# Kernel tuning notes

Hardware: AMD Instinct MI355X
Metric: run time of the kernel (lower is better)

Reference implementation:

```python
import jax, jax.numpy as jnp
import numpy as np

SR = 44100        # sample rate (init arg)
WIN = 442         # FFT window length from tensor[i:i+442]
HOP = 4           # loop stride
NBINS = 221       # kept spectrum bins x[:221]
THR = 0.01        # threshold passed to inner fftLayer
REL = 0.0594      # relative pitch-change threshold
BIN_HZ = 100.0    # argmax*100 -> frequency


def _windows_and_mag(tensor):
    n = tensor.shape[0]
    n_win = (n - WIN + HOP - 1) // HOP
    starts = jnp.arange(n_win) * HOP
    windows = tensor[starts[:, None] + jnp.arange(WIN)[None, :]]
    spec = jnp.fft.fft(windows, axis=-1)[:, :NBINS]           # complex64 [n_win, 221]
    spec = jnp.where(jnp.abs(spec) < THR, jnp.zeros_like(spec), spec)  # fftLayer threshold
    mag = jnp.abs(spec.real) + jnp.abs(spec.imag)             # |re| + |im|, as in forward
    return mag, starts


def setup_inputs() -> dict:
    key = jax.random.key(0)
    return {"tensor": jax.random.normal(key, (1_000_000,), dtype=jnp.float32)}


def reference(tensor):
    mag, starts = _windows_and_mag(tensor)
    # per-window dominant frequency: argmax bin * 100 Hz
    tmp = jnp.argmax(mag, axis=-1).astype(jnp.float32) * BIN_HZ    # [n_win]
    i_samp = starts.astype(jnp.float32)                            # sample index of each window

    def step(carry, x):
        maxF, Ftime = carry
        t, i = x
        cond = jnp.abs(maxF - t) > maxF * REL
        emit_f = maxF
        emit_d = (i - Ftime) * 1000.0 / SR
        maxF = jnp.where(cond, t, maxF)
        Ftime = jnp.where(cond, i, Ftime)
        return (maxF, Ftime), (cond, emit_f, emit_d)

    (maxF, Ftime), (flags, freqs, durs) = jax.lax.scan(
        step, (jnp.float32(0.0), jnp.float32(0.0)), (tmp, i_samp))
    # trailing append after the loop: (maxF, (i_last - Ftime)*1000/44100)
    final = jnp.stack([maxF, (i_samp[-1] - Ftime) * 1000.0 / SR])
    # flags marks windows where a note boundary was emitted; (freqs, durs) at those
    # positions are the (maxF, duration_ms) pairs the original appends to `out`.
    return flags, freqs, durs, final
```

## Files before the change

### kernel.cpp

```cpp
#include <hip/hip_runtime.h>

#define WIN 442
#define HOP 4
#define NBINS 221
#define LC 128
#define SPAN 960
#define B2 1024
#define NG 32

constexpr double kPI = 3.14159265358979323846264338327950288;

constexpr double tsin_poly(double r) {
    double t = r, s = r;
    for (int n = 1; n <= 9; ++n) { t *= -(r * r) / ((2.0 * n) * (2.0 * n + 1.0)); s += t; }
    return s;
}
constexpr double tcos_poly(double r) {
    double t = 1.0, c = 1.0;
    for (int n = 1; n <= 9; ++n) { t *= -(r * r) / ((2.0 * n - 1.0) * (2.0 * n)); c += t; }
    return c;
}
struct SC { double s, c; };
constexpr SC tsincos(double a) {
    int q = (int)(a / (kPI / 2) + 0.5);
    double r = a - q * (kPI / 2);
    double sr = tsin_poly(r), cr = tcos_poly(r);
    switch (q & 3) {
        case 0: return {sr, cr};
        case 1: return {cr, -sr};
        case 2: return {-sr, -cr};
        default: return {-cr, sr};
    }
}
struct TabF { float c[WIN]; float s[WIN]; };
constexpr TabF make_tabf() {
    TabF t{};
    for (int i = 0; i < WIN; ++i) {
        SC sc = tsincos(2.0 * kPI * (double)i / 442.0);
        t.c[i] = (float)sc.c; t.s[i] = (float)(-sc.s);
    }
    return t;
}
struct TabR { double c4[NBINS], s4[NBINS], c8[NBINS], s8[NBINS]; };
constexpr TabR make_tabr() {
    TabR t{};
    for (int k = 0; k < NBINS; ++k) {
        SC a = tsincos(2.0 * kPI * (double)((4 * k) % WIN) / 442.0);
        t.c4[k] = a.c; t.s4[k] = a.s;
        SC b = tsincos(2.0 * kPI * (double)((8 * k) % WIN) / 442.0);
        t.c8[k] = b.c; t.s8[k] = b.s;
    }
    return t;
}
__constant__ TabF cTabF = make_tabf();
__constant__ TabR cTabR = make_tabr();

static __device__ __forceinline__ unsigned long long shflx64(unsigned long long v, int off) {
    unsigned int lo = (unsigned int)v, hi = (unsigned int)(v >> 32);
    lo = __shfl_xor(lo, off, 64);
    hi = __shfl_xor(hi, off, 64);
    return ((unsigned long long)hi << 32) | lo;
}

__global__ __launch_bounds__(128) void k_slide(
    const float* __restrict__ x, int n, int n_win, int n_chunks,
    int* __restrict__ a_arr) {
    __shared__ __align__(16) float Xs[SPAN];
    __shared__ __align__(16) float Ds_[LC * 4];
    __shared__ unsigned long long cand[LC][9];

    const int tid = threadIdx.x;
    const int lane = tid & 63;
    const int wc = tid >> 6;
    const int chunk = blockIdx.x;
    const int s0 = chunk * (LC * HOP);

    for (int i = tid; i < SPAN; i += 128) {
        int g = s0 + i;
        Xs[i] = (g < n) ? x[g] : 0.0f;
    }
    __syncthreads();
    for (int r = tid; r < LC * 4; r += 128) Ds_[r] = Xs[r + WIN] - Xs[r];
    __syncthreads();

    const int wlen = min(LC, n_win - chunk * LC);

    const int k0 = lane + 128 * wc, k1 = k0 + 64;
    const bool a0 = (k0 < NBINS), a1 = (k1 < NBINS);
    const int kk0 = a0 ? k0 : 0, kk1 = a1 ? k1 : 0;
    const unsigned int lo0 = 255u - (unsigned)k0, lo1 = 255u - (unsigned)k1;

    float ec0[8], es0[8], ec1[8], es1[8];
    {
        int t0 = 0, t1 = 0;
#pragma unroll
        for (int m = 1; m < 8; ++m) {
            t0 += kk0; if (t0 >= WIN) t0 -= WIN;
            ec0[m] = cTabF.c[t0]; es0[m] = cTabF.s[t0];
            t1 += kk1; if (t1 >= WIN) t1 -= WIN;
            ec1[m] = cTabF.c[t1]; es1[m] = cTabF.s[t1];
        }
    }
    double C40 = a0 ? cTabR.c4[kk0] : 0.0, S40 = a0 ? cTabR.s4[kk0] : 0.0;
    double C41 = a1 ? cTabR.c4[kk1] : 0.0, S41 = a1 ? cTabR.s4[kk1] : 0.0;
    const double C80 = cTabR.c8[kk0], S80 = cTabR.s8[kk0];
    const double C81 = cTabR.c8[kk1], S81 = cTabR.s8[kk1];

    double S0r, S0i, S1r, S1i;
    {
        float xa = Xs[440], xb = Xs[441];
        S0r = (double)fmaf(xb, ec0[1], xa);
        S0i = (double)(xb * es0[1]);
        S1r = (double)fmaf(xb, ec1[1], xa);
        S1i = (double)(xb * es1[1]);
        const float4* Xq = (const float4*)Xs;
#pragma unroll 1
        for (int t = 54; t >= 0; --t) {
            float4 va = Xq[2 * t], vb = Xq[2 * t + 1];
            float Dr0 = va.x;
            Dr0 = fmaf(va.y, ec0[1], Dr0); Dr0 = fmaf(va.z, ec0[2], Dr0);
            Dr0 = fmaf(va.w, ec0[3], Dr0); Dr0 = fmaf(vb.x, ec0[4], Dr0);
            Dr0 = fmaf(vb.y, ec0[5], Dr0); Dr0 = fmaf(vb.z, ec0[6], Dr0);
            Dr0 = fmaf(vb.w, ec0[7], Dr0);
            float Di0 = va.y * es0[1];
            Di0 = fmaf(va.z, es0[2], Di0); Di0 = fmaf(va.w, es0[3], Di0);
            Di0 = fmaf(vb.x, es0[4], Di0); Di0 = fmaf(vb.y, es0[5], Di0);
            Di0 = fmaf(vb.z, es0[6], Di0); Di0 = fmaf(vb.w, es0[7], Di0);
            double nr = fma(S0r, C80, fma(S0i, S80, (double)Dr0));
            double ni = fma(S0i, C80, fma(S0r, -S80, (double)Di0));
            S0r = nr; S0i = ni;
            float Dr1 = va.x;
            Dr1 = fmaf(va.y, ec1[1], Dr1); Dr1 = fmaf(va.z, ec1[2], Dr1);
            Dr1 = fmaf(va.w, ec1[3], Dr1); Dr1 = fmaf(vb.x, ec1[4], Dr1);
            Dr1 = fmaf(vb.y, ec1[5], Dr1); Dr1 = fmaf(vb.z, ec1[6], Dr1);
            Dr1 = fmaf(vb.w, ec1[7], Dr1);
            float Di1 = va.y * es1[1];
            Di1 = fmaf(va.z, es1[2], Di1); Di1 = fmaf(va.w, es1[3], Di1);
            Di1 = fmaf(vb.x, es1[4], Di1); Di1 = fmaf(vb.y, es1[5], Di1);
            Di1 = fmaf(vb.z, es1[6], Di1); Di1 = fmaf(vb.w, es1[7], Di1);
            nr = fma(S1r, C81, fma(S1i, S81, (double)Dr1));
            ni = fma(S1i, C81, fma(S1r, -S81, (double)Di1));
            S1r = nr; S1i = ni;
        }
    }
    if (!a0) { S0r = 0.0; S0i = 0.0; }
    if (!a1) { S1r = 0.0; S1i = 0.0; }

    const float4* Dq = (const float4*)Ds_;
    for (int b = 0; b < 16; ++b) {
        unsigned long long key[8];
#pragma unroll
        for (int u = 0; u < 8; ++u) {
            if (b | u) {
                float4 d = Dq[b * 8 + u - 1];
                float Dr0 = fmaf(d.w, ec0[3], fmaf(d.z, ec0[2], fmaf(d.y, ec0[1], d.x)));
                float Di0 = fmaf(d.w, es0[3], fmaf(d.z, es0[2], d.y * es0[1]));
                double nr = S0r + (double)Dr0;
                double ni = S0i + (double)Di0;
                S0r = fma(nr, C40, -(ni * S40));
                S0i = fma(nr, S40, ni * C40);
                float Dr1 = fmaf(d.w, ec1[3], fmaf(d.z, ec1[2], fmaf(d.y, ec1[1], d.x)));
                float Di1 = fmaf(d.w, es1[3], fmaf(d.z, es1[2], d.y * es1[1]));
                nr = S1r + (double)Dr1;
                ni = S1i + (double)Di1;
                S1r = fma(nr, C41, -(ni * S41));
                S1i = fma(nr, S41, ni * C41);
            }
            float m0 = (float)(fabs(S0r) + fabs(S0i));
            float m1 = (float)(fabs(S1r) + fabs(S1i));
            unsigned long long key0 = ((unsigned long long)__float_as_uint(m0) << 32) | lo0;
            unsigned long long key1 = ((unsigned long long)__float_as_uint(m1) << 32) | lo1;
            key[u] = (key1 > key0) ? key1 : key0;
        }
#pragma unroll
        for (int s = 0; s < 4; ++s) {
            const int off = 32 >> s;
#pragma unroll
            for (int u = 0; u < 8; ++u) {
                unsigned long long o = shflx64(key[u], off);
                if (o > key[u]) key[u] = o;
            }
        }
        if (lane < 4) {
#pragma unroll
            for (int u = 0; u < 8; ++u) cand[b * 8 + u][wc * 4 + lane] = key[u];
        }
    }
    __syncthreads();
    if (tid < wlen) {
        unsigned long long best = cand[tid][0];
#pragma unroll
        for (int i = 1; i < 8; ++i) {
            unsigned long long c = cand[tid][i];
            if (c > best) best = c;
        }
        a_arr[chunk * LC + tid] = 255 - (int)(best & 255u);
    }
}

__global__ __launch_bounds__(256) void k_maps(const int* __restrict__ a_arr, int n_win,
                                              int L2, int* __restrict__ M0) {
    __shared__ float tf[256];
    __shared__ int ti[256];
    int j = blockIdx.x;
    int wbeg = j * L2;
    int cnt = n_win - wbeg; if (cnt > L2) cnt = L2; if (cnt < 0) cnt = 0;
    for (int i = threadIdx.x; i < cnt; i += 256) {
        int a = a_arr[wbeg + i];
        ti[i] = a; tf[i] = 100.0f * (float)a;
    }
    __syncthreads();
    int b = threadIdx.x;
    if (b < NBINS) {
        float mF = 100.0f * (float)b;
        int bin = b, rw = -1;
        for (int i = 0; i < cnt; ++i) {
            float t = tf[i];
            if (fabsf(mF - t) > mF * 0.0594f) { mF = t; bin = ti[i]; rw = wbeg + i; }
        }
        M0[j * NBINS + b] = ((rw + 1) << 8) | bin;
    }
}

__global__ __launch_bounds__(256) void k_sm1(const int* __restrict__ M0,
                                             int* __restrict__ M1) {
    __shared__ int sm[32 * NBINS];
    int g = blockIdx.x;
    for (int i = threadIdx.x; i < 32 * NBINS; i += 256) sm[i] = M0[g * 32 * NBINS + i];
    __syncthreads();
    int b = threadIdx.x;
    if (b < NBINS) {
        int bin = b, rw = -1;
        for (int i = 0; i < 32; ++i) {
            int mp = sm[i * NBINS + bin];
            if (mp >> 8) { rw = (mp >> 8) - 1; bin = mp & 255; }
        }
        M1[g * NBINS + b] = ((rw + 1) << 8) | bin;
    }
}

__global__ __launch_bounds__(256) void k_emit(const int* __restrict__ a_arr,
    const int* __restrict__ M0, const int* __restrict__ M1, int n_win, int L2,
    float* __restrict__ flags, float* __restrict__ freqs, float* __restrict__ durs,
    float* __restrict__ out_final) {
    __shared__ int sm1[NG * NBINS];
    __shared__ int sm0[32 * NBINS];
    __shared__ float tf[256];
    __shared__ int e0s;
    int j = blockIdx.x;
    int g = j >> 5;
    int wbeg = j * L2;
    int cnt = n_win - wbeg; if (cnt > L2) cnt = L2;
    if (cnt <= 0) return;
    for (int i = threadIdx.x; i < NG * NBINS; i += 256) sm1[i] = M1[i];
    for (int i = threadIdx.x; i < 32 * NBINS; i += 256) sm0[i] = M0[g * 32 * NBINS + i];
    for (int i = threadIdx.x; i < cnt; i += 256) tf[i] = 100.0f * (float)a_arr[wbeg + i];
    __syncthreads();
    if (threadIdx.x == 0) {
        int bin = 0, rw = -1;
        for (int i = 0; i < g; ++i) {
            int mp = sm1[i * NBINS + bin];
            if (mp >> 8) { rw = (mp >> 8) - 1; bin = mp & 255; }
        }
        int lim = j & 31;
        for (int i = 0; i < lim; ++i) {
            int mp = sm0[i * NBINS + bin];
            if (mp >> 8) { rw = (mp >> 8) - 1; bin = mp & 255; }
        }
        e0s = ((rw + 1) << 8) | bin;
    }
    __syncthreads();
    int t = threadIdx.x;
    if (t < cnt) {
        int st = e0s;
        float maxF = 100.0f * (float)(st & 255);
        int rw = (st >> 8) - 1;
        float Ftime = (rw < 0) ? 0.0f : 4.0f * (float)rw;
        for (int i = 0; i < t; ++i) {
            float tv = tf[i];
            if (fabsf(maxF - tv) > maxF * 0.0594f) {
                maxF = tv; Ftime = 4.0f * (float)(wbeg + i);
            }
        }
        int w = wbeg + t;
        float tv = tf[t];
        float iw = 4.0f * (float)w;
        bool cond = fabsf(maxF - tv) > maxF * 0.0594f;
        flags[w] = cond ? 1.0f : 0.0f;
        freqs[w] = maxF;
        durs[w] = (iw - Ftime) * 1000.0f / 44100.0f;
        if (w == n_win - 1) {
            float fMax = cond ? tv : maxF;
            float fT   = cond ? iw : Ftime;
            out_final[0] = fMax;
            out_final[1] = (iw - fT) * 1000.0f / 44100.0f;
        }
    }
}

extern "C" void kernel_launch(void* const* d_in, const int* in_sizes, int n_in,
                              void* d_out, int out_size, void* d_ws, size_t ws_size,
                              hipStream_t stream) {
    const float* x = (const float*)d_in[0];
    int n = in_sizes[0];
    int n_win = (n - WIN + HOP - 1) / HOP;
    float* out = (float*)d_out;
    char* ws = (char*)d_ws;

    int n_chunks = (n_win + LC - 1) / LC;
    int L2 = (n_win + B2 - 1) / B2;

    int* a_arr = (int*)(ws + 0);
    int* M0    = (int*)(ws + 1000448);
    int* M1    = (int*)(ws + 1905664);

    k_slide<<<dim3(n_chunks), dim3(128), 0, stream>>>(x, n, n_win, n_chunks, a_arr);
    k_maps<<<dim3(B2), dim3(256), 0, stream>>>(a_arr, n_win, L2, M0);
    k_sm1<<<dim3(NG), dim3(256), 0, stream>>>(M0, M1);
    k_emit<<<dim3(B2), dim3(256), 0, stream>>>(a_arr, M0, M1, n_win, L2,
                                               out, out + (size_t)n_win,
                                               out + 2 * (size_t)n_win,
                                               out + 3 * (size_t)n_win);
}
```

Measured before the change: 180.0 us.

## Fuse scan stages into one persistent kernel with grid barriers

Merges the three scan kernels (per-segment state maps, group composition, emission) into one kernel of 256 blocks that synchronises through atomic grid-wide barriers in workspace. Segments become larger (about 976 windows), so the emission phase loops over 256-window sub-tiles and carries state between them through shared memory. The intent is to remove kernel launch gaps and the redundant shared-memory loads of the map tables. In exchange it depends on all 256 blocks being co-resident for the spin barriers, adds a memset, and each thread's serial prefix loop still grows with the segment size.

```diff
diff --git a/kernel.cpp b/kernel.cpp
--- a/kernel.cpp
+++ b/kernel.cpp
@@ -5,8 +5,10 @@
 #define NBINS 221
 #define LC 128
 #define SPAN 960
-#define B2 1024
-#define NG 32
+#define B2 256
+#define GSZ 16
+#define NGRP 16
+#define SEGW_MAX 1024
 
 constexpr double kPI = 3.14159265358979323846264338327950288;
 
@@ -198,103 +200,101 @@
     }
 }
 
-__global__ __launch_bounds__(256) void k_maps(const int* __restrict__ a_arr, int n_win,
-                                              int L2, int* __restrict__ M0) {
-    __shared__ float tf[256];
-    __shared__ int ti[256];
-    int j = blockIdx.x;
-    int wbeg = j * L2;
-    int cnt = n_win - wbeg; if (cnt > L2) cnt = L2; if (cnt < 0) cnt = 0;
-    for (int i = threadIdx.x; i < cnt; i += 256) {
-        int a = a_arr[wbeg + i];
-        ti[i] = a; tf[i] = 100.0f * (float)a;
-    }
-    __syncthreads();
-    int b = threadIdx.x;
-    if (b < NBINS) {
-        float mF = 100.0f * (float)b;
-        int bin = b, rw = -1;
+__global__ __launch_bounds__(256) void k_scan(
+    const int* __restrict__ a_arr, int n_win, int segw,
+    int* __restrict__ M0, int* __restrict__ M1, unsigned int* __restrict__ bar,
+    float* __restrict__ flags, float* __restrict__ freqs, float* __restrict__ durs,
+    float* __restrict__ out_final) {
+    __shared__ float tf[SEGW_MAX];
+    __shared__ int smap[GSZ * NBINS];
+    __shared__ float sh_mF, sh_Ft;
+
+    const int j = blockIdx.x;
+    const int tid = threadIdx.x;
+    const int wbeg = j * segw;
+    int cnt = n_win - wbeg; if (cnt > segw) cnt = segw; if (cnt < 0) cnt = 0;
+
+    for (int i = tid; i < cnt; i += 256) tf[i] = 100.0f * (float)a_arr[wbeg + i];
+    __syncthreads();
+    if (tid < NBINS) {
+        float mF = 100.0f * (float)tid;
+        int rw = -1;
         for (int i = 0; i < cnt; ++i) {
             float t = tf[i];
-            if (fabsf(mF - t) > mF * 0.0594f) { mF = t; bin = ti[i]; rw = wbeg + i; }
-        }
-        M0[j * NBINS + b] = ((rw + 1) << 8) | bin;
-    }
-}
-
-__global__ __launch_bounds__(256) void k_sm1(const int* __restrict__ M0,
-                                             int* __restrict__ M1) {
-    __shared__ int sm[32 * NBINS];
-    int g = blockIdx.x;
-    for (int i = threadIdx.x; i < 32 * NBINS; i += 256) sm[i] = M0[g * 32 * NBINS + i];
-    __syncthreads();
-    int b = threadIdx.x;
-    if (b < NBINS) {
-        int bin = b, rw = -1;
-        for (int i = 0; i < 32; ++i) {
-            int mp = sm[i * NBINS + bin];
-            if (mp >> 8) { rw = (mp >> 8) - 1; bin = mp & 255; }
-        }
-        M1[g * NBINS + b] = ((rw + 1) << 8) | bin;
-    }
-}
-
-__global__ __launch_bounds__(256) void k_emit(const int* __restrict__ a_arr,
-    const int* __restrict__ M0, const int* __restrict__ M1, int n_win, int L2,
-    float* __restrict__ flags, float* __restrict__ freqs, float* __restrict__ durs,
-    float* __restrict__ out_final) {
-    __shared__ int sm1[NG * NBINS];
-    __shared__ int sm0[32 * NBINS];
-    __shared__ float tf[256];
-    __shared__ int e0s;
-    int j = blockIdx.x;
-    int g = j >> 5;
-    int wbeg = j * L2;
-    int cnt = n_win - wbeg; if (cnt > L2) cnt = L2;
-    if (cnt <= 0) return;
-    for (int i = threadIdx.x; i < NG * NBINS; i += 256) sm1[i] = M1[i];
-    for (int i = threadIdx.x; i < 32 * NBINS; i += 256) sm0[i] = M0[g * 32 * NBINS + i];
-    for (int i = threadIdx.x; i < cnt; i += 256) tf[i] = 100.0f * (float)a_arr[wbeg + i];
-    __syncthreads();
-    if (threadIdx.x == 0) {
+            if (fabsf(mF - t) > mF * 0.0594f) { mF = t; rw = wbeg + i; }
+        }
+        int bin = __float2int_rn(mF * 0.01f);
+        M0[j * NBINS + tid] = ((rw + 1) << 8) | bin;
+    }
+    __syncthreads();
+    if (tid == 0) {
+        __threadfence();
+        atomicAdd(&bar[0], 1u);
+        while (atomicAdd(&bar[0], 0u) < (unsigned)gridDim.x) __builtin_amdgcn_s_sleep(2);
+        __threadfence();
+    }
+    __syncthreads();
+    if (j < NGRP) {
+        for (int i = tid; i < GSZ * NBINS; i += 256) smap[i] = M0[j * GSZ * NBINS + i];
+        __syncthreads();
+        if (tid < NBINS) {
+            int bin = tid, rw = -1;
+            for (int i = 0; i < GSZ; ++i) {
+                int mp = smap[i * NBINS + bin];
+                if (mp >> 8) { rw = (mp >> 8) - 1; bin = mp & 255; }
+            }
+            M1[j * NBINS + tid] = ((rw + 1) << 8) | bin;
+        }
+    }
+    __syncthreads();
+    if (tid == 0) {
+        __threadfence();
+        atomicAdd(&bar[1], 1u);
+        while (atomicAdd(&bar[1], 0u) < (unsigned)gridDim.x) __builtin_amdgcn_s_sleep(2);
+        __threadfence();
+    }
+    __syncthreads();
+    if (tid == 0) {
+        int g = j / GSZ;
         int bin = 0, rw = -1;
         for (int i = 0; i < g; ++i) {
-            int mp = sm1[i * NBINS + bin];
+            int mp = M1[i * NBINS + bin];
             if (mp >> 8) { rw = (mp >> 8) - 1; bin = mp & 255; }
         }
-        int lim = j & 31;
-        for (int i = 0; i < lim; ++i) {
-            int mp = sm0[i * NBINS + bin];
+        for (int i = g * GSZ; i < j; ++i) {
+            int mp = M0[i * NBINS + bin];
             if (mp >> 8) { rw = (mp >> 8) - 1; bin = mp & 255; }
         }
-        e0s = ((rw + 1) << 8) | bin;
-    }
-    __syncthreads();
-    int t = threadIdx.x;
-    if (t < cnt) {
-        int st = e0s;
-        float maxF = 100.0f * (float)(st & 255);
-        int rw = (st >> 8) - 1;
-        float Ftime = (rw < 0) ? 0.0f : 4.0f * (float)rw;
-        for (int i = 0; i < t; ++i) {
-            float tv = tf[i];
-            if (fabsf(maxF - tv) > maxF * 0.0594f) {
-                maxF = tv; Ftime = 4.0f * (float)(wbeg + i);
-            }
-        }
-        int w = wbeg + t;
-        float tv = tf[t];
-        float iw = 4.0f * (float)w;
-        bool cond = fabsf(maxF - tv) > maxF * 0.0594f;
-        flags[w] = cond ? 1.0f : 0.0f;
-        freqs[w] = maxF;
-        durs[w] = (iw - Ftime) * 1000.0f / 44100.0f;
-        if (w == n_win - 1) {
-            float fMax = cond ? tv : maxF;
-            float fT   = cond ? iw : Ftime;
-            out_final[0] = fMax;
-            out_final[1] = (iw - fT) * 1000.0f / 44100.0f;
-        }
+        sh_mF = 100.0f * (float)bin;
+        sh_Ft = (rw < 0) ? 0.0f : 4.0f * (float)rw;
+    }
+    __syncthreads();
+    for (int t0 = 0; t0 < cnt; t0 += 256) {
+        int tcnt = cnt - t0; if (tcnt > 256) tcnt = 256;
+        float mF = sh_mF, Ft = sh_Ft;
+        __syncthreads();
+        if (tid < tcnt) {
+            for (int i = 0; i < tid; ++i) {
+                float tv = tf[t0 + i];
+                if (fabsf(mF - tv) > mF * 0.0594f) {
+                    mF = tv; Ft = 4.0f * (float)(wbeg + t0 + i);
+                }
+            }
+            int w = wbeg + t0 + tid;
+            float tv = tf[t0 + tid];
+            float iw = 4.0f * (float)w;
+            bool cond = fabsf(mF - tv) > mF * 0.0594f;
+            flags[w] = cond ? 1.0f : 0.0f;
+            freqs[w] = mF;
+            durs[w] = (iw - Ft) * 1000.0f / 44100.0f;
+            if (cond) { mF = tv; Ft = iw; }
+            if (tid == tcnt - 1) { sh_mF = mF; sh_Ft = Ft; }
+            if (w == n_win - 1) {
+                out_final[0] = mF;
+                out_final[1] = (iw - Ft) * 1000.0f / 44100.0f;
+            }
+        }
+        __syncthreads();
     }
 }
 
@@ -308,16 +308,16 @@
     char* ws = (char*)d_ws;
 
     int n_chunks = (n_win + LC - 1) / LC;
-    int L2 = (n_win + B2 - 1) / B2;
-
-    int* a_arr = (int*)(ws + 0);
-    int* M0    = (int*)(ws + 1000448);
-    int* M1    = (int*)(ws + 1905664);
-
+    int segw = (n_win + B2 - 1) / B2;
+
+    int* a_arr        = (int*)(ws + 0);
+    int* M0           = (int*)(ws + 1000448);
+    int* M1           = (int*)(ws + 1226752);
+    unsigned int* bar = (unsigned int*)(ws + 1240896);
+
+    hipMemsetAsync(bar, 0, 8, stream);
     k_slide<<<dim3(n_chunks), dim3(128), 0, stream>>>(x, n, n_win, n_chunks, a_arr);
-    k_maps<<<dim3(B2), dim3(256), 0, stream>>>(a_arr, n_win, L2, M0);
-    k_sm1<<<dim3(NG), dim3(256), 0, stream>>>(M0, M1);
-    k_emit<<<dim3(B2), dim3(256), 0, stream>>>(a_arr, M0, M1, n_win, L2,
+    k_scan<<<dim3(B2), dim3(256), 0, stream>>>(a_arr, n_win, segw, M0, M1, bar,
                                                out, out + (size_t)n_win,
                                                out + 2 * (size_t)n_win,
                                                out + 3 * (size_t)n_win);
```

Result: slower. 216.3 us (+20.2%).

## Fuse per-chunk state-map build into sliding DFT kernel and precompute chunk seeds

Applied to the files above, without the earlier changes.

The per-bin state-transition maps are now built inside k_slide over each 128-window chunk, which removes the separate k_maps pass. The maps are stored as 16-bit entries, and a new k_e0 kernel computes each chunk's starting state once, so k_emit no longer redoes a serial prefix walk per block. The emit stage now runs with 128-thread blocks, one per chunk. The final shuffle reduction also stops one step earlier and merges 16 candidates per window in shared memory. In exchange, k_slide does extra serial map-building work, and there are many more chunk-level maps to compose (about 1953 chunks in 62 groups).

```diff
diff --git a/kernel.cpp b/kernel.cpp
--- a/kernel.cpp
+++ b/kernel.cpp
@@ -5,8 +5,7 @@
 #define NBINS 221
 #define LC 128
 #define SPAN 960
-#define B2 1024
-#define NG 32
+#define GSZ 32
 
 constexpr double kPI = 3.14159265358979323846264338327950288;
 
@@ -64,10 +63,10 @@
 
 __global__ __launch_bounds__(128) void k_slide(
     const float* __restrict__ x, int n, int n_win, int n_chunks,
-    int* __restrict__ a_arr) {
+    int* __restrict__ a_arr, unsigned short* __restrict__ M0) {
     __shared__ __align__(16) float Xs[SPAN];
     __shared__ __align__(16) float Ds_[LC * 4];
-    __shared__ unsigned long long cand[LC][9];
+    __shared__ unsigned long long cand[LC][17];
 
     const int tid = threadIdx.x;
     const int lane = tid & 63;
@@ -173,7 +172,7 @@
             key[u] = (key1 > key0) ? key1 : key0;
         }
 #pragma unroll
-        for (int s = 0; s < 4; ++s) {
+        for (int s = 0; s < 3; ++s) {
             const int off = 32 >> s;
 #pragma unroll
             for (int u = 0; u < 8; ++u) {
@@ -181,98 +180,99 @@
                 if (o > key[u]) key[u] = o;
             }
         }
-        if (lane < 4) {
-#pragma unroll
-            for (int u = 0; u < 8; ++u) cand[b * 8 + u][wc * 4 + lane] = key[u];
-        }
-    }
-    __syncthreads();
+        if (lane < 8) {
+#pragma unroll
+            for (int u = 0; u < 8; ++u) cand[b * 8 + u][wc * 8 + lane] = key[u];
+        }
+    }
+    __syncthreads();
+    int* ti = (int*)Ds_;
+    float* tfl = Ds_ + LC;
     if (tid < wlen) {
         unsigned long long best = cand[tid][0];
 #pragma unroll
-        for (int i = 1; i < 8; ++i) {
+        for (int i = 1; i < 16; ++i) {
             unsigned long long c = cand[tid][i];
             if (c > best) best = c;
         }
-        a_arr[chunk * LC + tid] = 255 - (int)(best & 255u);
-    }
-}
-
-__global__ __launch_bounds__(256) void k_maps(const int* __restrict__ a_arr, int n_win,
-                                              int L2, int* __restrict__ M0) {
-    __shared__ float tf[256];
-    __shared__ int ti[256];
-    int j = blockIdx.x;
-    int wbeg = j * L2;
-    int cnt = n_win - wbeg; if (cnt > L2) cnt = L2; if (cnt < 0) cnt = 0;
-    for (int i = threadIdx.x; i < cnt; i += 256) {
-        int a = a_arr[wbeg + i];
-        ti[i] = a; tf[i] = 100.0f * (float)a;
-    }
-    __syncthreads();
-    int b = threadIdx.x;
-    if (b < NBINS) {
+        int a = 255 - (int)(best & 255u);
+        a_arr[chunk * LC + tid] = a;
+        ti[tid] = a;
+        tfl[tid] = 100.0f * (float)a;
+    }
+    __syncthreads();
+    for (int b = tid; b < NBINS; b += 128) {
         float mF = 100.0f * (float)b;
-        int bin = b, rw = -1;
-        for (int i = 0; i < cnt; ++i) {
-            float t = tf[i];
-            if (fabsf(mF - t) > mF * 0.0594f) { mF = t; bin = ti[i]; rw = wbeg + i; }
-        }
-        M0[j * NBINS + b] = ((rw + 1) << 8) | bin;
-    }
-}
-
-__global__ __launch_bounds__(256) void k_sm1(const int* __restrict__ M0,
-                                             int* __restrict__ M1) {
-    __shared__ int sm[32 * NBINS];
+        int bin = b, rel = -1;
+        for (int i = 0; i < wlen; ++i) {
+            float t = tfl[i];
+            if (fabsf(mF - t) > mF * 0.0594f) { mF = t; bin = ti[i]; rel = i; }
+        }
+        M0[chunk * NBINS + b] = (unsigned short)(((rel + 1) << 8) | bin);
+    }
+}
+
+__global__ __launch_bounds__(256) void k_sm1(const unsigned short* __restrict__ M0,
+                                             int n_chunks, int* __restrict__ M1) {
+    __shared__ unsigned short sm[GSZ * NBINS];
     int g = blockIdx.x;
-    for (int i = threadIdx.x; i < 32 * NBINS; i += 256) sm[i] = M0[g * 32 * NBINS + i];
+    int c0 = g * GSZ;
+    int cn = min(GSZ, n_chunks - c0);
+    for (int i = threadIdx.x; i < cn * NBINS; i += 256) sm[i] = M0[c0 * NBINS + i];
     __syncthreads();
     int b = threadIdx.x;
     if (b < NBINS) {
         int bin = b, rw = -1;
-        for (int i = 0; i < 32; ++i) {
-            int mp = sm[i * NBINS + bin];
+        for (int i = 0; i < cn; ++i) {
+            unsigned short mp = sm[i * NBINS + bin];
+            if (mp >> 8) { rw = (c0 + i) * LC + (int)(mp >> 8) - 1; bin = mp & 255; }
+        }
+        M1[g * NBINS + b] = ((rw + 1) << 8) | bin;
+    }
+}
+
+__global__ __launch_bounds__(256) void k_e0(const unsigned short* __restrict__ M0,
+                                            const int* __restrict__ M1,
+                                            int n_chunks, int ngrp,
+                                            int* __restrict__ E0) {
+    extern __shared__ char dyn[];
+    int* m1s = (int*)dyn;
+    unsigned short* m0s = (unsigned short*)(m1s + ngrp * NBINS);
+    int g = blockIdx.x;
+    int c0 = g * GSZ;
+    int cn = min(GSZ, n_chunks - c0);
+    for (int i = threadIdx.x; i < ngrp * NBINS; i += 256) m1s[i] = M1[i];
+    for (int i = threadIdx.x; i < cn * NBINS; i += 256) m0s[i] = M0[c0 * NBINS + i];
+    __syncthreads();
+    int j = threadIdx.x;
+    if (j < cn) {
+        int bin = 0, rw = -1;
+        for (int i = 0; i < g; ++i) {
+            int mp = m1s[i * NBINS + bin];
             if (mp >> 8) { rw = (mp >> 8) - 1; bin = mp & 255; }
         }
-        M1[g * NBINS + b] = ((rw + 1) << 8) | bin;
-    }
-}
-
-__global__ __launch_bounds__(256) void k_emit(const int* __restrict__ a_arr,
-    const int* __restrict__ M0, const int* __restrict__ M1, int n_win, int L2,
+        for (int q = 0; q < j; ++q) {
+            unsigned short mp = m0s[q * NBINS + bin];
+            if (mp >> 8) { rw = (c0 + q) * LC + (int)(mp >> 8) - 1; bin = mp & 255; }
+        }
+        E0[c0 + j] = ((rw + 1) << 8) | bin;
+    }
+}
+
+__global__ __launch_bounds__(128) void k_emit(const int* __restrict__ a_arr,
+    const int* __restrict__ E0, int n_win,
     float* __restrict__ flags, float* __restrict__ freqs, float* __restrict__ durs,
     float* __restrict__ out_final) {
-    __shared__ int sm1[NG * NBINS];
-    __shared__ int sm0[32 * NBINS];
-    __shared__ float tf[256];
-    __shared__ int e0s;
+    __shared__ float tf[LC];
     int j = blockIdx.x;
-    int g = j >> 5;
-    int wbeg = j * L2;
-    int cnt = n_win - wbeg; if (cnt > L2) cnt = L2;
+    int wbeg = j * LC;
+    int cnt = n_win - wbeg; if (cnt > LC) cnt = LC;
     if (cnt <= 0) return;
-    for (int i = threadIdx.x; i < NG * NBINS; i += 256) sm1[i] = M1[i];
-    for (int i = threadIdx.x; i < 32 * NBINS; i += 256) sm0[i] = M0[g * 32 * NBINS + i];
-    for (int i = threadIdx.x; i < cnt; i += 256) tf[i] = 100.0f * (float)a_arr[wbeg + i];
-    __syncthreads();
-    if (threadIdx.x == 0) {
-        int bin = 0, rw = -1;
-        for (int i = 0; i < g; ++i) {
-            int mp = sm1[i * NBINS + bin];
-            if (mp >> 8) { rw = (mp >> 8) - 1; bin = mp & 255; }
-        }
-        int lim = j & 31;
-        for (int i = 0; i < lim; ++i) {
-            int mp = sm0[i * NBINS + bin];
-            if (mp >> 8) { rw = (mp >> 8) - 1; bin = mp & 255; }
-        }
-        e0s = ((rw + 1) << 8) | bin;
-    }
+    for (int i = threadIdx.x; i < cnt; i += 128) tf[i] = 100.0f * (float)a_arr[wbeg + i];
     __syncthreads();
     int t = threadIdx.x;
     if (t < cnt) {
-        int st = e0s;
+        int st = E0[j];
         float maxF = 100.0f * (float)(st & 255);
         int rw = (st >> 8) - 1;
         float Ftime = (rw < 0) ? 0.0f : 4.0f * (float)rw;
@@ -308,17 +308,20 @@
     char* ws = (char*)d_ws;
 
     int n_chunks = (n_win + LC - 1) / LC;
-    int L2 = (n_win + B2 - 1) / B2;
-
-    int* a_arr = (int*)(ws + 0);
-    int* M0    = (int*)(ws + 1000448);
-    int* M1    = (int*)(ws + 1905664);
-
-    k_slide<<<dim3(n_chunks), dim3(128), 0, stream>>>(x, n, n_win, n_chunks, a_arr);
-    k_maps<<<dim3(B2), dim3(256), 0, stream>>>(a_arr, n_win, L2, M0);
-    k_sm1<<<dim3(NG), dim3(256), 0, stream>>>(M0, M1);
-    k_emit<<<dim3(B2), dim3(256), 0, stream>>>(a_arr, M0, M1, n_win, L2,
-                                               out, out + (size_t)n_win,
-                                               out + 2 * (size_t)n_win,
-                                               out + 3 * (size_t)n_win);
-}
+    int ngrp = (n_chunks + GSZ - 1) / GSZ;
+
+    int* a_arr         = (int*)(ws + 0);
+    unsigned short* M0 = (unsigned short*)(ws + 1000448);
+    int* M1            = (int*)(ws + 1864192);
+    int* E0            = (int*)(ws + 1919232);
+
+    size_t e0_lds = (size_t)ngrp * NBINS * 4 + (size_t)GSZ * NBINS * 2;
+
+    k_slide<<<dim3(n_chunks), dim3(128), 0, stream>>>(x, n, n_win, n_chunks, a_arr, M0);
+    k_sm1<<<dim3(ngrp), dim3(256), 0, stream>>>(M0, n_chunks, M1);
+    k_e0<<<dim3(ngrp), dim3(256), e0_lds, stream>>>(M0, M1, n_chunks, ngrp, E0);
+    k_emit<<<dim3(n_chunks), dim3(128), 0, stream>>>(a_arr, E0, n_win,
+                                                     out, out + (size_t)n_win,
+                                                     out + 2 * (size_t)n_win,
+                                                     out + 3 * (size_t)n_win);
+}
```

After: 193.3 us. +7.4%, slower.
